# Kernel tuning notes

Hardware: AMD Instinct MI355X
Metric: run time of the kernel (lower is better)

The kernel has to match this reference:

```python
import jax, jax.numpy as jnp
import numpy as np

V_A, V_HP = 256, 256
H_A, H_HP = 2048, 4096
DEPTH = 12


def lstm_cell(x, h, c, W_ih, W_hh, b_ih, b_hh):
    # PyTorch LSTM cell: gate order i, f, g, o along the 4H axis.
    gates = x @ W_ih.T + h @ W_hh.T + (b_ih + b_hh)
    i, f, g, o = jnp.split(gates, 4, axis=-1)
    c_new = jax.nn.sigmoid(f) * c + jax.nn.sigmoid(i) * jnp.tanh(g)
    h_new = jax.nn.sigmoid(o) * jnp.tanh(c_new)
    return h_new, c_new


def setup_inputs() -> dict:
    key = jax.random.key(0)
    ks = jax.random.split(key, 16)
    s = jnp.float32(0.02)
    f32 = jnp.float32
    return {
        "x_thought_vec_arch": jax.random.normal(ks[0], (1, 1, H_A), f32),
        "x_thought_vec_arch_hp": jax.random.normal(ks[1], (1, 1, H_HP), f32),
        # arch LSTM (input V_A, hidden H_A)
        "W_ih_a": jax.random.normal(ks[2], (4 * H_A, V_A), f32) * s,
        "W_hh_a": jax.random.normal(ks[3], (4 * H_A, H_A), f32) * s,
        "b_ih_a": jax.random.normal(ks[4], (4 * H_A,), f32) * s,
        "b_hh_a": jax.random.normal(ks[5], (4 * H_A,), f32) * s,
        # arch_out Linear (H_A -> V_A)
        "W_out_a": jax.random.normal(ks[6], (V_A, H_A), f32) * s,
        "b_out_a": jax.random.normal(ks[7], (V_A,), f32) * s,
        # hp_summarizer Linear (H_HP -> H_HP//2)
        "W_sum": jax.random.normal(ks[8], (H_HP // 2, H_HP), f32) * s,
        "b_sum": jax.random.normal(ks[9], (H_HP // 2,), f32) * s,
        # arch_hp LSTM (input V_A + V_HP, hidden H_HP)
        "W_ih_hp": jax.random.normal(ks[10], (4 * H_HP, V_A + V_HP), f32) * s,
        "W_hh_hp": jax.random.normal(ks[11], (4 * H_HP, H_HP), f32) * s,
        "b_ih_hp": jax.random.normal(ks[12], (4 * H_HP,), f32) * s,
        "b_hh_hp": jax.random.normal(ks[13], (4 * H_HP,), f32) * s,
        # arch_hp_out Linear (H_HP -> V_HP)
        "W_out_hp": jax.random.normal(ks[14], (V_HP, H_HP), f32) * s,
        "b_out_hp": jax.random.normal(ks[15], (V_HP,), f32) * s,
    }


def reference(x_thought_vec_arch, x_thought_vec_arch_hp,
              W_ih_a, W_hh_a, b_ih_a, b_hh_a, W_out_a, b_out_a,
              W_sum, b_sum, W_ih_hp, W_hh_hp, b_ih_hp, b_hh_hp,
              W_out_hp, b_out_hp):
    h_a, h_hp = x_thought_vec_arch, x_thought_vec_arch_hp  # thought vecs used as hidden states
    c_a = jnp.zeros_like(h_a)
    c_hp = jnp.zeros_like(h_hp)
    a = jnp.full((1, 1, V_A), 1.0 / V_A, jnp.float32)       # SOS soft one-hot
    a_hp = jnp.full((1, 1, V_HP), 1.0 / V_HP, jnp.float32)

    def step(carry, _):
        a, a_hp, h_a, c_a, h_hp, c_hp = carry
        # forward_arch: seq_len=1 so LSTM output == new hidden
        h_a, c_a = lstm_cell(a, h_a, c_a, W_ih_a, W_hh_a, b_ih_a, b_hh_a)
        a = jax.nn.softmax(h_a @ W_out_a.T + b_out_a, axis=-1)
        # forward_arch_hp (keeps the original's swapped hx=(c_hp, prev_h_hp)):
        h_sum = jax.nn.relu(h_hp @ W_sum.T + b_sum)
        prev_h_hp = jnp.concatenate([h_a, h_sum], axis=-1)   # used as CELL state
        inp = jnp.concatenate([a, a_hp], axis=-1)
        h_hp, c_hp = lstm_cell(inp, c_hp, prev_h_hp, W_ih_hp, W_hh_hp, b_ih_hp, b_hh_hp)
        a_hp = jax.nn.softmax(h_hp @ W_out_hp.T + b_out_hp, axis=-1)
        return (a, a_hp, h_a, c_a, h_hp, c_hp), (a, a_hp)

    _, (ys_a, ys_hp) = jax.lax.scan(step, (a, a_hp, h_a, c_a, h_hp, c_hp), None, length=DEPTH)
    # torch.cat(list_of_(1,1,V), dim=1) -> (1, DEPTH, V)
    arch = ys_a.reshape(DEPTH, V_A)[None]
    arch_hp = ys_hp.reshape(DEPTH, V_HP)[None]
    return arch, arch_hp
```

## Files before the change

kernel.cpp:

```cpp
#include <hip/hip_runtime.h>
#include <hip/hip_fp16.h>

#define H_A   2048
#define H_HP  4096
#define V_A   256
#define V_HP  256
#define DEPTH 12

struct Half8 { __half2 a, b, c, d; };
struct Half4 { __half2 a, b; };

__device__ __forceinline__ float sigmoidf_(float x) { return 1.0f / (1.0f + expf(-x)); }

__device__ __forceinline__ float dot4_(float4 a, float4 b) {
    return a.x * b.x + a.y * b.y + a.z * b.z + a.w * b.w;
}

__device__ __forceinline__ float dot8h_(Half8 w, float4 x0, float4 x1) {
    float2 wa = __half22float2(w.a), wb = __half22float2(w.b);
    float2 wc = __half22float2(w.c), wd = __half22float2(w.d);
    return wa.x * x0.x + wa.y * x0.y + wb.x * x0.z + wb.y * x0.w +
           wc.x * x1.x + wc.y * x1.y + wd.x * x1.z + wd.y * x1.w;
}

__device__ __forceinline__ float waveReduceSum(float v) {
#pragma unroll
    for (int off = 32; off > 0; off >>= 1) v += __shfl_xor(v, off, 64);
    return v;
}

__global__ __launch_bounds__(256) void k_f2h(const float* __restrict__ src,
                                             __half* __restrict__ dst, int n8)
{
    int i = blockIdx.x * 256 + threadIdx.x;
    if (i < n8) {
        float4 a = ((const float4*)src)[2 * i];
        float4 b = ((const float4*)src)[2 * i + 1];
        Half8 h;
        h.a = __floats2half2_rn(a.x, a.y);
        h.b = __floats2half2_rn(a.z, a.w);
        h.c = __floats2half2_rn(b.x, b.y);
        h.d = __floats2half2_rn(b.z, b.w);
        ((Half8*)dst)[i] = h;
    }
}

__global__ void k_init(const float* __restrict__ x_a, const float* __restrict__ x_hp,
                       float* __restrict__ h_a, float* __restrict__ c_a0,
                       float* __restrict__ h_hp, float* __restrict__ c_hp,
                       float* __restrict__ a_vec, float* __restrict__ logits_hp)
{
    int i = blockIdx.x * 256 + threadIdx.x;
    if (i < H_A)  { h_a[i] = x_a[i];  c_a0[i] = 0.0f; }
    if (i < H_HP) { h_hp[i] = x_hp[i]; c_hp[i] = 0.0f; }
    if (i < V_A)  { a_vec[i] = 1.0f / 256.0f; logits_hp[i] = 0.0f; }
}

__global__ __launch_bounds__(256) void k1_fused_gemv(
    const __half* __restrict__ hW_ih_a, const __half* __restrict__ hW_hh_a,
    const float* __restrict__ b_ih_a, const float* __restrict__ b_hh_a,
    const __half* __restrict__ hW_sum,  const float* __restrict__ b_sum,
    const __half* __restrict__ hW_hh_hp, const float* __restrict__ b_ih_hp,
    const float* __restrict__ b_hh_hp,
    const float* __restrict__ a_vec,  const float* __restrict__ h_a,
    const float* __restrict__ h_hp,   const float* __restrict__ c_hp,
    float* __restrict__ gates_a, float* __restrict__ h_sum_o,
    float* __restrict__ gacc_hp, int skip_c)
{
    const int lane = threadIdx.x & 63;
    const int wave = (blockIdx.x << 2) | (threadIdx.x >> 6);

    if (wave < 8192) {
        const int r = wave;
        Half4 w = ((const Half4*)(hW_ih_a + (size_t)r * V_A))[lane];
        float4 x = ((const float4*)a_vec)[lane];
        float2 w0 = __half22float2(w.a), w1 = __half22float2(w.b);
        float acc = w0.x * x.x + w0.y * x.y + w1.x * x.z + w1.y * x.w;
        const Half8* wh = (const Half8*)(hW_hh_a + (size_t)r * H_A);
        const float4* xh = (const float4*)h_a;
#pragma unroll
        for (int it = 0; it < 4; ++it) {
            int idx = it * 64 + lane;
            acc += dot8h_(wh[idx], xh[2 * idx], xh[2 * idx + 1]);
        }
        acc = waveReduceSum(acc);
        if (lane == 0) gates_a[r] = acc + b_ih_a[r] + b_hh_a[r];
    } else if (wave < 10240) {
        const int r = wave - 8192;
        const Half8* ww = (const Half8*)(hW_sum + (size_t)r * H_HP);
        const float4* xx = (const float4*)h_hp;
        float acc = 0.0f;
#pragma unroll
        for (int it = 0; it < 8; ++it) {
            int idx = it * 64 + lane;
            acc += dot8h_(ww[idx], xx[2 * idx], xx[2 * idx + 1]);
        }
        acc = waveReduceSum(acc);
        if (lane == 0) h_sum_o[r] = fmaxf(acc + b_sum[r], 0.0f);
    } else {
        const int r = wave - 10240;
        float acc = 0.0f;
        if (!skip_c) {
            const Half8* ww = (const Half8*)(hW_hh_hp + (size_t)r * H_HP);
            const float4* xx = (const float4*)c_hp;
#pragma unroll
            for (int it = 0; it < 8; ++it) {
                int idx = it * 64 + lane;
                acc += dot8h_(ww[idx], xx[2 * idx], xx[2 * idx + 1]);
            }
            acc = waveReduceSum(acc);
        }
        if (lane == 0) gacc_hp[r] = acc + b_ih_hp[r] + b_hh_hp[r];
    }
}

__global__ __launch_bounds__(256) void k3_arch(
    const float* __restrict__ gates_a, const float* __restrict__ c_in,
    float* __restrict__ c_out, float* __restrict__ h_a_g,
    const float* __restrict__ W_out_a, const float* __restrict__ b_out_a,
    float* __restrict__ logits_a)
{
    __shared__ float h_s[H_A];
    const int t = threadIdx.x;
#pragma unroll
    for (int k = 0; k < 8; ++k) {
        int e = t + k * 256;
        float gi = gates_a[e];
        float gf = gates_a[H_A + e];
        float gg = gates_a[2 * H_A + e];
        float go = gates_a[3 * H_A + e];
        float c_new = sigmoidf_(gf) * c_in[e] + sigmoidf_(gi) * tanhf(gg);
        float h = sigmoidf_(go) * tanhf(c_new);
        h_s[e] = h;
        if (blockIdx.x == 0) { c_out[e] = c_new; h_a_g[e] = h; }
    }
    __syncthreads();
    const int lane = t & 63;
    const int r = (blockIdx.x << 2) | (t >> 6);
    const float4* w4 = (const float4*)(W_out_a + (size_t)r * H_A);
    const float4* h4 = (const float4*)h_s;
    float acc = 0.0f;
#pragma unroll
    for (int it = 0; it < 8; ++it) {
        acc += dot4_(w4[it * 64 + lane], h4[it * 64 + lane]);
    }
    acc = waveReduceSum(acc);
    if (lane == 0) logits_a[r] = acc + b_out_a[r];
}

__device__ __forceinline__ void softmax256_dev(const float* __restrict__ logits,
                                               float* __restrict__ vec,
                                               float* __restrict__ outp)
{
    __shared__ float sh[4];
    const int t = threadIdx.x;
    const int lane = t & 63, wv = t >> 6;
    float v = logits[t];
    float m = v;
#pragma unroll
    for (int off = 32; off > 0; off >>= 1) m = fmaxf(m, __shfl_xor(m, off, 64));
    if (lane == 0) sh[wv] = m;
    __syncthreads();
    m = fmaxf(fmaxf(sh[0], sh[1]), fmaxf(sh[2], sh[3]));
    __syncthreads();
    float e = expf(v - m);
    float s = waveReduceSum(e);
    if (lane == 0) sh[wv] = s;
    __syncthreads();
    s = sh[0] + sh[1] + sh[2] + sh[3];
    __syncthreads();
    float p = e / s;
    vec[t] = p;
    outp[t] = p;
}

__global__ __launch_bounds__(256) void k4_softmax2(
    const float* __restrict__ logits_a, float* __restrict__ a_vec,
    float* __restrict__ out_a,
    const float* __restrict__ logits_hp, float* __restrict__ ahp_vec,
    float* __restrict__ out_hp)
{
    softmax256_dev(logits_a, a_vec, out_a);
    __syncthreads();
    softmax256_dev(logits_hp, ahp_vec, out_hp);
}

__global__ __launch_bounds__(256) void k_softmax_tail(
    const float* __restrict__ logits_hp, float* __restrict__ ahp_vec,
    float* __restrict__ outp)
{
    softmax256_dev(logits_hp, ahp_vec, outp);
}

__global__ __launch_bounds__(256) void k5_ih_hp(
    const __half* __restrict__ hW_ih_hp, const float* __restrict__ a_vec,
    const float* __restrict__ ahp_vec, float* __restrict__ gacc_hp)
{
    const int lane = threadIdx.x & 63;
    const int r = (blockIdx.x << 2) | (threadIdx.x >> 6);
    Half8 w = ((const Half8*)(hW_ih_hp + (size_t)r * (V_A + V_HP)))[lane];
    const float* xv = (lane < 32) ? (a_vec + 8 * lane) : (ahp_vec + 8 * lane - 256);
    float4 x0 = ((const float4*)xv)[0];
    float4 x1 = ((const float4*)xv)[1];
    float acc = dot8h_(w, x0, x1);
    acc = waveReduceSum(acc);
    if (lane == 0) gacc_hp[r] += acc;
}

__global__ __launch_bounds__(256) void k6_hp_point(
    const float* __restrict__ gacc_hp, const float* __restrict__ h_a,
    const float* __restrict__ h_sum, float* __restrict__ c_hp,
    float* __restrict__ h_hp)
{
    int e = blockIdx.x * 256 + threadIdx.x;
    float gi = gacc_hp[e];
    float gf = gacc_hp[H_HP + e];
    float gg = gacc_hp[2 * H_HP + e];
    float go = gacc_hp[3 * H_HP + e];
    float prev = (e < H_A) ? h_a[e] : h_sum[e - H_A];
    float c = sigmoidf_(gf) * prev + sigmoidf_(gi) * tanhf(gg);
    float h = sigmoidf_(go) * tanhf(c);
    c_hp[e] = c;
    h_hp[e] = h;
}

__global__ __launch_bounds__(256) void k7_out_hp(
    const float* __restrict__ W_out_hp, const float* __restrict__ b_out_hp,
    const float* __restrict__ h_hp, float* __restrict__ logits_hp)
{
    const int lane = threadIdx.x & 63;
    const int r = (blockIdx.x << 2) | (threadIdx.x >> 6);
    const float4* w4 = (const float4*)(W_out_hp + (size_t)r * H_HP);
    const float4* x4 = (const float4*)h_hp;
    float acc = 0.0f;
#pragma unroll 4
    for (int it = 0; it < 16; ++it) {
        acc += dot4_(w4[it * 64 + lane], x4[it * 64 + lane]);
    }
    acc = waveReduceSum(acc);
    if (lane == 0) logits_hp[r] = acc + b_out_hp[r];
}


extern "C" void kernel_launch(void* const* d_in, const int* in_sizes, int n_in,
                              void* d_out, int out_size, void* d_ws, size_t ws_size,
                              hipStream_t stream)
{
    const float* x_a      = (const float*)d_in[0];
    const float* x_hp     = (const float*)d_in[1];
    const float* W_ih_a   = (const float*)d_in[2];
    const float* W_hh_a   = (const float*)d_in[3];
    const float* b_ih_a   = (const float*)d_in[4];
    const float* b_hh_a   = (const float*)d_in[5];
    const float* W_out_a  = (const float*)d_in[6];
    const float* b_out_a  = (const float*)d_in[7];
    const float* W_sum    = (const float*)d_in[8];
    const float* b_sum    = (const float*)d_in[9];
    const float* W_ih_hp  = (const float*)d_in[10];
    const float* W_hh_hp  = (const float*)d_in[11];
    const float* b_ih_hp  = (const float*)d_in[12];
    const float* b_hh_hp  = (const float*)d_in[13];
    const float* W_out_hp = (const float*)d_in[14];
    const float* b_out_hp = (const float*)d_in[15];

    float* out = (float*)d_out;

    __half* hW_ih_a  = (__half*)d_ws;
    __half* hW_hh_a  = hW_ih_a + 2097152;
    __half* hW_sum   = hW_hh_a + 16777216;
    __half* hW_ih_hp = hW_sum + 8388608;
    __half* hW_hh_hp = hW_ih_hp + 8388608;
    float* ws = (float*)(hW_hh_hp + 67108864);

    float* gates_a   = ws;
    float* h_sum     = ws + 8192;
    float* gacc_hp   = ws + 10240;
    float* h_a       = ws + 26624;
    float* c_a0      = ws + 28672;
    float* c_a1      = ws + 30720;
    float* h_hp      = ws + 32768;
    float* c_hp      = ws + 36864;
    float* logits_a  = ws + 40960;
    float* logits_hp = ws + 41216;
    float* a_vec     = ws + 41472;
    float* ahp_vec   = ws + 41728;
    float* dummy     = ws + 41984;
    float* c_a[2]    = { c_a0, c_a1 };

    k_f2h<<<(2097152 / 8 + 255) / 256, 256, 0, stream>>>(W_ih_a, hW_ih_a, 2097152 / 8);
    k_f2h<<<(16777216 / 8 + 255) / 256, 256, 0, stream>>>(W_hh_a, hW_hh_a, 16777216 / 8);
    k_f2h<<<(8388608 / 8 + 255) / 256, 256, 0, stream>>>(W_sum, hW_sum, 8388608 / 8);
    k_f2h<<<(8388608 / 8 + 255) / 256, 256, 0, stream>>>(W_ih_hp, hW_ih_hp, 8388608 / 8);
    k_f2h<<<(67108864 / 8 + 255) / 256, 256, 0, stream>>>(W_hh_hp, hW_hh_hp, 67108864 / 8);

    k_init<<<16, 256, 0, stream>>>(x_a, x_hp, h_a, c_a0, h_hp, c_hp, a_vec, logits_hp);

    for (int t = 0; t < DEPTH; ++t) {
        k1_fused_gemv<<<6656, 256, 0, stream>>>(
            hW_ih_a, hW_hh_a, b_ih_a, b_hh_a, hW_sum, b_sum,
            hW_hh_hp, b_ih_hp, b_hh_hp,
            a_vec, h_a, h_hp, c_hp,
            gates_a, h_sum, gacc_hp, (t == 0) ? 1 : 0);

        k3_arch<<<64, 256, 0, stream>>>(gates_a, c_a[t & 1], c_a[(t + 1) & 1], h_a,
                                        W_out_a, b_out_a, logits_a);

        k4_softmax2<<<1, 256, 0, stream>>>(
            logits_a, a_vec, out + (size_t)t * V_A,
            logits_hp, ahp_vec,
            (t == 0) ? dummy : out + (size_t)DEPTH * V_A + (size_t)(t - 1) * V_HP);

        k5_ih_hp<<<4096, 256, 0, stream>>>(hW_ih_hp, a_vec, ahp_vec, gacc_hp);

        k6_hp_point<<<16, 256, 0, stream>>>(gacc_hp, h_a, h_sum, c_hp, h_hp);

        k7_out_hp<<<64, 256, 0, stream>>>(W_out_hp, b_out_hp, h_hp, logits_hp);
    }

    k_softmax_tail<<<1, 256, 0, stream>>>(
        logits_hp, ahp_vec, out + (size_t)DEPTH * V_A + (size_t)(DEPTH - 1) * V_HP);
}
```

Baseline: 1.088 ms.

## Fuse per-step kernels, batch weight conversion, fold W_hh_hp cast into step 0

```diff
diff --git a/kernel.cpp b/kernel.cpp
--- a/kernel.cpp
+++ b/kernel.cpp
@@ -8,12 +8,10 @@
 #define DEPTH 12
 
 struct Half8 { __half2 a, b, c, d; };
-struct Half4 { __half2 a, b; };
-
-__device__ __forceinline__ float sigmoidf_(float x) { return 1.0f / (1.0f + expf(-x)); }
-
-__device__ __forceinline__ float dot4_(float4 a, float4 b) {
-    return a.x * b.x + a.y * b.y + a.z * b.z + a.w * b.w;
+
+__device__ __forceinline__ float fsig_(float x) { return 1.0f / (1.0f + __expf(-x)); }
+__device__ __forceinline__ float ftanh_(float x) {
+    return 1.0f - 2.0f / (__expf(2.0f * x) + 1.0f);
 }
 
 __device__ __forceinline__ float dot8h_(Half8 w, float4 x0, float4 x1) {
@@ -23,26 +21,19 @@
            wc.x * x1.x + wc.y * x1.y + wd.x * x1.z + wd.y * x1.w;
 }
 
+__device__ __forceinline__ Half8 cvt8_(float4 a, float4 b) {
+    Half8 h;
+    h.a = __floats2half2_rn(a.x, a.y);
+    h.b = __floats2half2_rn(a.z, a.w);
+    h.c = __floats2half2_rn(b.x, b.y);
+    h.d = __floats2half2_rn(b.z, b.w);
+    return h;
+}
+
 __device__ __forceinline__ float waveReduceSum(float v) {
 #pragma unroll
     for (int off = 32; off > 0; off >>= 1) v += __shfl_xor(v, off, 64);
     return v;
-}
-
-__global__ __launch_bounds__(256) void k_f2h(const float* __restrict__ src,
-                                             __half* __restrict__ dst, int n8)
-{
-    int i = blockIdx.x * 256 + threadIdx.x;
-    if (i < n8) {
-        float4 a = ((const float4*)src)[2 * i];
-        float4 b = ((const float4*)src)[2 * i + 1];
-        Half8 h;
-        h.a = __floats2half2_rn(a.x, a.y);
-        h.b = __floats2half2_rn(a.z, a.w);
-        h.c = __floats2half2_rn(b.x, b.y);
-        h.d = __floats2half2_rn(b.z, b.w);
-        ((Half8*)dst)[i] = h;
-    }
 }
 
 __global__ void k_init(const float* __restrict__ x_a, const float* __restrict__ x_hp,
@@ -56,25 +47,49 @@
     if (i < V_A)  { a_vec[i] = 1.0f / 256.0f; logits_hp[i] = 0.0f; }
 }
 
-__global__ __launch_bounds__(256) void k1_fused_gemv(
+__global__ __launch_bounds__(256) void k_f2h_batched(
+    const float* __restrict__ W_ih_a,  __half* __restrict__ hW_ih_a,
+    const float* __restrict__ W_hh_a,  __half* __restrict__ hW_hh_a,
+    const float* __restrict__ W_sum,   __half* __restrict__ hW_sum,
+    const float* __restrict__ W_ih_hp, __half* __restrict__ hW_ih_hp,
+    const float* __restrict__ W_out_a, __half* __restrict__ hW_out_a,
+    const float* __restrict__ W_out_hp,__half* __restrict__ hW_out_hp)
+{
+    int i = blockIdx.x * 256 + threadIdx.x;
+    const float* src; __half* dst; int base;
+    if      (i < 262144)  { src = W_ih_a;   dst = hW_ih_a;   base = 0; }
+    else if (i < 2359296) { src = W_hh_a;   dst = hW_hh_a;   base = 262144; }
+    else if (i < 3407872) { src = W_sum;    dst = hW_sum;    base = 2359296; }
+    else if (i < 4456448) { src = W_ih_hp;  dst = hW_ih_hp;  base = 3407872; }
+    else if (i < 4521984) { src = W_out_a;  dst = hW_out_a;  base = 4456448; }
+    else if (i < 4653056) { src = W_out_hp; dst = hW_out_hp; base = 4521984; }
+    else return;
+    int j = i - base;
+    float4 a = ((const float4*)src)[2 * j];
+    float4 b = ((const float4*)src)[2 * j + 1];
+    ((Half8*)dst)[j] = cvt8_(a, b);
+}
+
+__global__ __launch_bounds__(256) void kA_fused_gemv(
     const __half* __restrict__ hW_ih_a, const __half* __restrict__ hW_hh_a,
     const float* __restrict__ b_ih_a, const float* __restrict__ b_hh_a,
     const __half* __restrict__ hW_sum,  const float* __restrict__ b_sum,
-    const __half* __restrict__ hW_hh_hp, const float* __restrict__ b_ih_hp,
-    const float* __restrict__ b_hh_hp,
+    __half* __restrict__ hW_hh_hp, const float* __restrict__ W_hh_hp_f32,
+    const float* __restrict__ b_ih_hp, const float* __restrict__ b_hh_hp,
     const float* __restrict__ a_vec,  const float* __restrict__ h_a,
     const float* __restrict__ h_hp,   const float* __restrict__ c_hp,
     float* __restrict__ gates_a, float* __restrict__ h_sum_o,
-    float* __restrict__ gacc_hp, int skip_c)
+    float* __restrict__ gacc_hp, int step0)
 {
     const int lane = threadIdx.x & 63;
     const int wave = (blockIdx.x << 2) | (threadIdx.x >> 6);
 
     if (wave < 8192) {
         const int r = wave;
-        Half4 w = ((const Half4*)(hW_ih_a + (size_t)r * V_A))[lane];
+        const __half2* wp = (const __half2*)(hW_ih_a + (size_t)r * V_A);
+        __half2 w0h = wp[2 * lane], w1h = wp[2 * lane + 1];
         float4 x = ((const float4*)a_vec)[lane];
-        float2 w0 = __half22float2(w.a), w1 = __half22float2(w.b);
+        float2 w0 = __half22float2(w0h), w1 = __half22float2(w1h);
         float acc = w0.x * x.x + w0.y * x.y + w1.x * x.z + w1.y * x.w;
         const Half8* wh = (const Half8*)(hW_hh_a + (size_t)r * H_A);
         const float4* xh = (const float4*)h_a;
@@ -99,25 +114,34 @@
         if (lane == 0) h_sum_o[r] = fmaxf(acc + b_sum[r], 0.0f);
     } else {
         const int r = wave - 10240;
-        float acc = 0.0f;
-        if (!skip_c) {
+        if (step0) {
+            const float4* src = (const float4*)(W_hh_hp_f32 + (size_t)r * H_HP);
+            Half8* dst = (Half8*)(hW_hh_hp + (size_t)r * H_HP);
+#pragma unroll
+            for (int it = 0; it < 8; ++it) {
+                int idx = it * 64 + lane;
+                dst[idx] = cvt8_(src[2 * idx], src[2 * idx + 1]);
+            }
+            if (lane == 0) gacc_hp[r] = b_ih_hp[r] + b_hh_hp[r];
+        } else {
             const Half8* ww = (const Half8*)(hW_hh_hp + (size_t)r * H_HP);
             const float4* xx = (const float4*)c_hp;
+            float acc = 0.0f;
 #pragma unroll
             for (int it = 0; it < 8; ++it) {
                 int idx = it * 64 + lane;
                 acc += dot8h_(ww[idx], xx[2 * idx], xx[2 * idx + 1]);
             }
             acc = waveReduceSum(acc);
+            if (lane == 0) gacc_hp[r] = acc + b_ih_hp[r] + b_hh_hp[r];
         }
-        if (lane == 0) gacc_hp[r] = acc + b_ih_hp[r] + b_hh_hp[r];
-    }
-}
-
-__global__ __launch_bounds__(256) void k3_arch(
+    }
+}
+
+__global__ __launch_bounds__(256) void kB_arch(
     const float* __restrict__ gates_a, const float* __restrict__ c_in,
     float* __restrict__ c_out, float* __restrict__ h_a_g,
-    const float* __restrict__ W_out_a, const float* __restrict__ b_out_a,
+    const __half* __restrict__ hW_out_a, const float* __restrict__ b_out_a,
     float* __restrict__ logits_a)
 {
     __shared__ float h_s[H_A];
@@ -129,116 +153,131 @@
         float gf = gates_a[H_A + e];
         float gg = gates_a[2 * H_A + e];
         float go = gates_a[3 * H_A + e];
-        float c_new = sigmoidf_(gf) * c_in[e] + sigmoidf_(gi) * tanhf(gg);
-        float h = sigmoidf_(go) * tanhf(c_new);
+        float c_new = fsig_(gf) * c_in[e] + fsig_(gi) * ftanh_(gg);
+        float h = fsig_(go) * ftanh_(c_new);
         h_s[e] = h;
         if (blockIdx.x == 0) { c_out[e] = c_new; h_a_g[e] = h; }
     }
     __syncthreads();
     const int lane = t & 63;
     const int r = (blockIdx.x << 2) | (t >> 6);
-    const float4* w4 = (const float4*)(W_out_a + (size_t)r * H_A);
+    const Half8* w8 = (const Half8*)(hW_out_a + (size_t)r * H_A);
     const float4* h4 = (const float4*)h_s;
     float acc = 0.0f;
 #pragma unroll
-    for (int it = 0; it < 8; ++it) {
-        acc += dot4_(w4[it * 64 + lane], h4[it * 64 + lane]);
+    for (int it = 0; it < 4; ++it) {
+        int idx = it * 64 + lane;
+        acc += dot8h_(w8[idx], h4[2 * idx], h4[2 * idx + 1]);
     }
     acc = waveReduceSum(acc);
     if (lane == 0) logits_a[r] = acc + b_out_a[r];
 }
 
-__device__ __forceinline__ void softmax256_dev(const float* __restrict__ logits,
-                                               float* __restrict__ vec,
-                                               float* __restrict__ outp)
-{
-    __shared__ float sh[4];
+__global__ __launch_bounds__(256) void kC_softmax_ih(
+    const float* __restrict__ logits_a, const float* __restrict__ logits_hp,
+    const __half* __restrict__ hW_ih_hp, float* __restrict__ gacc_hp,
+    float* __restrict__ a_vec_g, float* __restrict__ out_a,
+    float* __restrict__ out_hp)
+{
+    __shared__ float p_all[512];
+    __shared__ float red[8];
+    const int t = threadIdx.x, lane = t & 63, wv = t >> 6;
+    float la = logits_a[t], lh = logits_hp[t];
+    float ma = la, mh = lh;
+#pragma unroll
+    for (int off = 32; off > 0; off >>= 1) {
+        ma = fmaxf(ma, __shfl_xor(ma, off, 64));
+        mh = fmaxf(mh, __shfl_xor(mh, off, 64));
+    }
+    if (lane == 0) { red[wv] = ma; red[4 + wv] = mh; }
+    __syncthreads();
+    ma = fmaxf(fmaxf(red[0], red[1]), fmaxf(red[2], red[3]));
+    mh = fmaxf(fmaxf(red[4], red[5]), fmaxf(red[6], red[7]));
+    __syncthreads();
+    float ea = __expf(la - ma), eh = __expf(lh - mh);
+    float sa = waveReduceSum(ea), sh = waveReduceSum(eh);
+    if (lane == 0) { red[wv] = sa; red[4 + wv] = sh; }
+    __syncthreads();
+    sa = red[0] + red[1] + red[2] + red[3];
+    sh = red[4] + red[5] + red[6] + red[7];
+    float pa = ea / sa, ph = eh / sh;
+    p_all[t] = pa;
+    p_all[256 + t] = ph;
+    if (blockIdx.x == 0) {
+        a_vec_g[t] = pa;
+        out_a[t] = pa;
+        out_hp[t] = ph;
+    }
+    __syncthreads();
+    const float4* x4 = (const float4*)p_all;
+    float4 xa = x4[2 * lane], xb = x4[2 * lane + 1];
+    const int gw = (blockIdx.x << 2) | wv;
+#pragma unroll
+    for (int rr = 0; rr < 4; ++rr) {
+        int r = (gw << 2) | rr;
+        Half8 w = ((const Half8*)(hW_ih_hp + (size_t)r * (V_A + V_HP)))[lane];
+        float acc = dot8h_(w, xa, xb);
+        acc = waveReduceSum(acc);
+        if (lane == 0) gacc_hp[r] += acc;
+    }
+}
+
+__global__ __launch_bounds__(256) void kD_hp(
+    const float* __restrict__ gacc_hp, const float* __restrict__ h_a,
+    const float* __restrict__ h_sum, float* __restrict__ c_hp_g,
+    float* __restrict__ h_hp_g,
+    const __half* __restrict__ hW_out_hp, const float* __restrict__ b_out_hp,
+    float* __restrict__ logits_hp)
+{
+    __shared__ float h_s[H_HP];
     const int t = threadIdx.x;
-    const int lane = t & 63, wv = t >> 6;
-    float v = logits[t];
-    float m = v;
-#pragma unroll
-    for (int off = 32; off > 0; off >>= 1) m = fmaxf(m, __shfl_xor(m, off, 64));
-    if (lane == 0) sh[wv] = m;
-    __syncthreads();
-    m = fmaxf(fmaxf(sh[0], sh[1]), fmaxf(sh[2], sh[3]));
-    __syncthreads();
-    float e = expf(v - m);
-    float s = waveReduceSum(e);
-    if (lane == 0) sh[wv] = s;
-    __syncthreads();
-    s = sh[0] + sh[1] + sh[2] + sh[3];
-    __syncthreads();
-    float p = e / s;
-    vec[t] = p;
-    outp[t] = p;
-}
-
-__global__ __launch_bounds__(256) void k4_softmax2(
-    const float* __restrict__ logits_a, float* __restrict__ a_vec,
-    float* __restrict__ out_a,
-    const float* __restrict__ logits_hp, float* __restrict__ ahp_vec,
-    float* __restrict__ out_hp)
-{
-    softmax256_dev(logits_a, a_vec, out_a);
-    __syncthreads();
-    softmax256_dev(logits_hp, ahp_vec, out_hp);
-}
-
-__global__ __launch_bounds__(256) void k_softmax_tail(
-    const float* __restrict__ logits_hp, float* __restrict__ ahp_vec,
-    float* __restrict__ outp)
-{
-    softmax256_dev(logits_hp, ahp_vec, outp);
-}
-
-__global__ __launch_bounds__(256) void k5_ih_hp(
-    const __half* __restrict__ hW_ih_hp, const float* __restrict__ a_vec,
-    const float* __restrict__ ahp_vec, float* __restrict__ gacc_hp)
-{
-    const int lane = threadIdx.x & 63;
-    const int r = (blockIdx.x << 2) | (threadIdx.x >> 6);
-    Half8 w = ((const Half8*)(hW_ih_hp + (size_t)r * (V_A + V_HP)))[lane];
-    const float* xv = (lane < 32) ? (a_vec + 8 * lane) : (ahp_vec + 8 * lane - 256);
-    float4 x0 = ((const float4*)xv)[0];
-    float4 x1 = ((const float4*)xv)[1];
-    float acc = dot8h_(w, x0, x1);
-    acc = waveReduceSum(acc);
-    if (lane == 0) gacc_hp[r] += acc;
-}
-
-__global__ __launch_bounds__(256) void k6_hp_point(
-    const float* __restrict__ gacc_hp, const float* __restrict__ h_a,
-    const float* __restrict__ h_sum, float* __restrict__ c_hp,
-    float* __restrict__ h_hp)
-{
-    int e = blockIdx.x * 256 + threadIdx.x;
-    float gi = gacc_hp[e];
-    float gf = gacc_hp[H_HP + e];
-    float gg = gacc_hp[2 * H_HP + e];
-    float go = gacc_hp[3 * H_HP + e];
-    float prev = (e < H_A) ? h_a[e] : h_sum[e - H_A];
-    float c = sigmoidf_(gf) * prev + sigmoidf_(gi) * tanhf(gg);
-    float h = sigmoidf_(go) * tanhf(c);
-    c_hp[e] = c;
-    h_hp[e] = h;
-}
-
-__global__ __launch_bounds__(256) void k7_out_hp(
-    const float* __restrict__ W_out_hp, const float* __restrict__ b_out_hp,
-    const float* __restrict__ h_hp, float* __restrict__ logits_hp)
-{
-    const int lane = threadIdx.x & 63;
-    const int r = (blockIdx.x << 2) | (threadIdx.x >> 6);
-    const float4* w4 = (const float4*)(W_out_hp + (size_t)r * H_HP);
-    const float4* x4 = (const float4*)h_hp;
+#pragma unroll
+    for (int k = 0; k < 16; ++k) {
+        int e = t + k * 256;
+        float gi = gacc_hp[e];
+        float gf = gacc_hp[H_HP + e];
+        float gg = gacc_hp[2 * H_HP + e];
+        float go = gacc_hp[3 * H_HP + e];
+        float prev = (e < H_A) ? h_a[e] : h_sum[e - H_A];
+        float c = fsig_(gf) * prev + fsig_(gi) * ftanh_(gg);
+        float h = fsig_(go) * ftanh_(c);
+        h_s[e] = h;
+        if (blockIdx.x == 0) { c_hp_g[e] = c; h_hp_g[e] = h; }
+    }
+    __syncthreads();
+    const int lane = t & 63;
+    const int r = (blockIdx.x << 2) | (t >> 6);
+    const Half8* w8 = (const Half8*)(hW_out_hp + (size_t)r * H_HP);
+    const float4* x4 = (const float4*)h_s;
     float acc = 0.0f;
-#pragma unroll 4
-    for (int it = 0; it < 16; ++it) {
-        acc += dot4_(w4[it * 64 + lane], x4[it * 64 + lane]);
+#pragma unroll
+    for (int it = 0; it < 8; ++it) {
+        int idx = it * 64 + lane;
+        acc += dot8h_(w8[idx], x4[2 * idx], x4[2 * idx + 1]);
     }
     acc = waveReduceSum(acc);
     if (lane == 0) logits_hp[r] = acc + b_out_hp[r];
+}
+
+__global__ __launch_bounds__(256) void k_softmax_tail(
+    const float* __restrict__ logits_hp, float* __restrict__ outp)
+{
+    __shared__ float red[4];
+    const int t = threadIdx.x, lane = t & 63, wv = t >> 6;
+    float v = logits_hp[t];
+    float m = v;
+#pragma unroll
+    for (int off = 32; off > 0; off >>= 1) m = fmaxf(m, __shfl_xor(m, off, 64));
+    if (lane == 0) red[wv] = m;
+    __syncthreads();
+    m = fmaxf(fmaxf(red[0], red[1]), fmaxf(red[2], red[3]));
+    __syncthreads();
+    float e = __expf(v - m);
+    float s = waveReduceSum(e);
+    if (lane == 0) red[wv] = s;
+    __syncthreads();
+    s = red[0] + red[1] + red[2] + red[3];
+    outp[t] = e / s;
 }
 
 
@@ -265,12 +304,14 @@
 
     float* out = (float*)d_out;
 
-    __half* hW_ih_a  = (__half*)d_ws;
-    __half* hW_hh_a  = hW_ih_a + 2097152;
-    __half* hW_sum   = hW_hh_a + 16777216;
-    __half* hW_ih_hp = hW_sum + 8388608;
-    __half* hW_hh_hp = hW_ih_hp + 8388608;
-    float* ws = (float*)(hW_hh_hp + 67108864);
+    __half* hW_ih_a   = (__half*)d_ws;
+    __half* hW_hh_a   = hW_ih_a   + 2097152;
+    __half* hW_sum    = hW_hh_a   + 16777216;
+    __half* hW_ih_hp  = hW_sum    + 8388608;
+    __half* hW_hh_hp  = hW_ih_hp  + 8388608;
+    __half* hW_out_a  = hW_hh_hp  + 67108864;
+    __half* hW_out_hp = hW_out_a  + 524288;
+    float* ws = (float*)(hW_out_hp + 1048576);
 
     float* gates_a   = ws;
     float* h_sum     = ws + 8192;
@@ -283,40 +324,34 @@
     float* logits_a  = ws + 40960;
     float* logits_hp = ws + 41216;
     float* a_vec     = ws + 41472;
-    float* ahp_vec   = ws + 41728;
-    float* dummy     = ws + 41984;
+    float* dummy     = ws + 41728;
     float* c_a[2]    = { c_a0, c_a1 };
 
-    k_f2h<<<(2097152 / 8 + 255) / 256, 256, 0, stream>>>(W_ih_a, hW_ih_a, 2097152 / 8);
-    k_f2h<<<(16777216 / 8 + 255) / 256, 256, 0, stream>>>(W_hh_a, hW_hh_a, 16777216 / 8);
-    k_f2h<<<(8388608 / 8 + 255) / 256, 256, 0, stream>>>(W_sum, hW_sum, 8388608 / 8);
-    k_f2h<<<(8388608 / 8 + 255) / 256, 256, 0, stream>>>(W_ih_hp, hW_ih_hp, 8388608 / 8);
-    k_f2h<<<(67108864 / 8 + 255) / 256, 256, 0, stream>>>(W_hh_hp, hW_hh_hp, 67108864 / 8);
-
     k_init<<<16, 256, 0, stream>>>(x_a, x_hp, h_a, c_a0, h_hp, c_hp, a_vec, logits_hp);
 
+    k_f2h_batched<<<18176, 256, 0, stream>>>(
+        W_ih_a, hW_ih_a, W_hh_a, hW_hh_a, W_sum, hW_sum,
+        W_ih_hp, hW_ih_hp, W_out_a, hW_out_a, W_out_hp, hW_out_hp);
+
     for (int t = 0; t < DEPTH; ++t) {
-        k1_fused_gemv<<<6656, 256, 0, stream>>>(
+        kA_fused_gemv<<<6656, 256, 0, stream>>>(
             hW_ih_a, hW_hh_a, b_ih_a, b_hh_a, hW_sum, b_sum,
-            hW_hh_hp, b_ih_hp, b_hh_hp,
+            hW_hh_hp, W_hh_hp, b_ih_hp, b_hh_hp,
             a_vec, h_a, h_hp, c_hp,
             gates_a, h_sum, gacc_hp, (t == 0) ? 1 : 0);
 
-        k3_arch<<<64, 256, 0, stream>>>(gates_a, c_a[t & 1], c_a[(t + 1) & 1], h_a,
-                                        W_out_a, b_out_a, logits_a);
-
-        k4_softmax2<<<1, 256, 0, stream>>>(
-            logits_a, a_vec, out + (size_t)t * V_A,
-            logits_hp, ahp_vec,
+        kB_arch<<<64, 256, 0, stream>>>(gates_a, c_a[t & 1], c_a[(t + 1) & 1], h_a,
+                                        hW_out_a, b_out_a, logits_a);
+
+        kC_softmax_ih<<<1024, 256, 0, stream>>>(
+            logits_a, logits_hp, hW_ih_hp, gacc_hp,
+            a_vec, out + (size_t)t * V_A,
             (t == 0) ? dummy : out + (size_t)DEPTH * V_A + (size_t)(t - 1) * V_HP);
 
-        k5_ih_hp<<<4096, 256, 0, stream>>>(hW_ih_hp, a_vec, ahp_vec, gacc_hp);
-
-        k6_hp_point<<<16, 256, 0, stream>>>(gacc_hp, h_a, h_sum, c_hp, h_hp);
-
-        k7_out_hp<<<64, 256, 0, stream>>>(W_out_hp, b_out_hp, h_hp, logits_hp);
+        kD_hp<<<64, 256, 0, stream>>>(gacc_hp, h_a, h_sum, c_hp, h_hp,
+                                      hW_out_hp, b_out_hp, logits_hp);
     }
 
     k_softmax_tail<<<1, 256, 0, stream>>>(
-        logits_hp, ahp_vec, out + (size_t)DEPTH * V_A + (size_t)(DEPTH - 1) * V_HP);
-}
+        logits_hp, out + (size_t)DEPTH * V_A + (size_t)(DEPTH - 1) * V_HP);
+}
```

Result: slower. 1.137 ms (+4.5%).
